# Kernel optimization log

Measured on AMD Instinct MI355X. Metric: run time of the kernel, lower is better.

Reference implementation:

```python
import jax, jax.numpy as jnp
import numpy as np
import math

D_MODEL = 768
NUM_HEADS = 12
D_K = D_MODEL // NUM_HEADS

def setup_inputs() -> dict:
    key = jax.random.key(0)
    k_x, k_q, k_k, k_v, k_o = jax.random.split(key, 5)
    x = jax.random.normal(k_x, (2, 2048, D_MODEL), dtype=jnp.float32)
    std = math.sqrt(2.0 / (D_MODEL + D_MODEL))
    # trunc_normal approx: clip normal to [-3std, 3std]
    def tn(k):
        return jnp.clip(jax.random.normal(k, (D_MODEL, D_MODEL), dtype=jnp.float32) * std, -3 * std, 3 * std)
    return {
        "x": x,
        "weight_query": tn(k_q),
        "weight_key": tn(k_k),
        "weight_value": tn(k_v),
        "weight_output": tn(k_o),
    }

def reference(x, weight_query, weight_key, weight_value, weight_output):
    # x: (b, s, d_model); weights: (d_out, d_model)
    b, s, _ = x.shape
    def proj_heads(w):
        y = jnp.einsum('od,bsd->bso', w, x)  # (b, s, h*dk)
        return y.reshape(b, s, NUM_HEADS, D_K).transpose(0, 2, 1, 3)  # (b, h, s, dk)
    Q = proj_heads(weight_query)
    K = proj_heads(weight_key)
    V = proj_heads(weight_value)
    scores = jnp.einsum('bhqd,bhkd->bhqk', Q, K) / jnp.sqrt(jnp.asarray(D_K, x.dtype))
    causal = jnp.tril(jnp.ones((s, s), dtype=bool))  # (sq, sk)
    scores = jnp.where(causal, scores, -jnp.inf)
    attn = jax.nn.softmax(scores, axis=-1)
    out_heads = jnp.einsum('bhqk,bhkd->bhqd', attn, V)  # (b, h, s, dv)
    attn_out = out_heads.transpose(0, 2, 1, 3).reshape(b, s, NUM_HEADS * D_K)
    return jnp.einsum('di,bsi->bsd', weight_output, attn_out)
```

## Files before the change

kernel.cpp:

```cpp
#include <hip/hip_runtime.h>
#include <stdint.h>

typedef float f32x4 __attribute__((ext_vector_type(4)));
typedef __bf16 bf16x8 __attribute__((ext_vector_type(8)));
typedef uint32_t u32a  __attribute__((may_alias));
typedef uint2    u2a   __attribute__((may_alias));
typedef uint4    u4a   __attribute__((may_alias));

#define VS 2064

__device__ __forceinline__ ushort f2b(float f) {
  uint32_t u = __builtin_bit_cast(uint32_t, f);
  u += 0x7FFFu + ((u >> 16) & 1u);
  return (ushort)(u >> 16);
}
__device__ __forceinline__ uint32_t b16(uint32_t u) {
  u += 0x7FFFu + ((u >> 16) & 1u);
  return u >> 16;
}

__device__ __forceinline__ bf16x8 ld_frag(const ushort* p) {
  u4a u = *(const u4a*)p;
  return __builtin_bit_cast(bf16x8, u);
}

__device__ __forceinline__ u4a cvt8(const float* p) {
  u4a a = *(const u4a*)p, b = *(const u4a*)(p + 4), o;
  o.x = b16(a.x) | (b16(a.y) << 16);
  o.y = b16(a.z) | (b16(a.w) << 16);
  o.z = b16(b.x) | (b16(b.y) << 16);
  o.w = b16(b.z) | (b16(b.w) << 16);
  return o;
}

__device__ __forceinline__ void load_lds16(const void* g, void* l) {
  __builtin_amdgcn_global_load_lds(
      (const __attribute__((address_space(1))) uint32_t*)g,
      (__attribute__((address_space(3))) uint32_t*)l, 16, 0, 0);
}

__device__ __forceinline__ uint32_t comb4(uint32_t a, uint32_t b, uint32_t c, uint32_t d,
                                          float w0, float w1, float w2, float w3) {
  float lo = __builtin_bit_cast(float, a << 16) * w0 +
             __builtin_bit_cast(float, b << 16) * w1 +
             __builtin_bit_cast(float, c << 16) * w2 +
             __builtin_bit_cast(float, d << 16) * w3;
  float hi = __builtin_bit_cast(float, a & 0xFFFF0000u) * w0 +
             __builtin_bit_cast(float, b & 0xFFFF0000u) * w1 +
             __builtin_bit_cast(float, c & 0xFFFF0000u) * w2 +
             __builtin_bit_cast(float, d & 0xFFFF0000u) * w3;
  return (uint32_t)f2b(lo) | ((uint32_t)f2b(hi) << 16);
}

__global__ __launch_bounds__(256) void convert_kernel(
    const float* __restrict__ x,  const float* __restrict__ wq,
    const float* __restrict__ wk, const float* __restrict__ wv,
    const float* __restrict__ wo,
    ushort* __restrict__ xb,  ushort* __restrict__ wqb,
    ushort* __restrict__ wkb, ushort* __restrict__ wvb,
    ushort* __restrict__ wob)
{
  const size_t NX = 3145728, NW = 589824;
  size_t idx = ((size_t)blockIdx.x * 256 + threadIdx.x) * 8;
  const float* src; ushort* dst; size_t off;
  if      (idx < NX)          { src = x;  dst = xb;  off = idx; }
  else if (idx < NX + NW)     { src = wq; dst = wqb; off = idx - NX; }
  else if (idx < NX + 2 * NW) { src = wk; dst = wkb; off = idx - NX - NW; }
  else if (idx < NX + 3 * NW) { src = wv; dst = wvb; off = idx - NX - 2 * NW; }
  else                        { src = wo; dst = wob; off = idx - NX - 3 * NW; }
  *(u4a*)(dst + off) = cvt8(src + off);
}

__global__ __launch_bounds__(256) void gemm_qkv(
    const ushort* __restrict__ A,
    const ushort* __restrict__ B0, const ushort* __restrict__ B1,
    const ushort* __restrict__ B2,
    ushort* __restrict__ Qo, ushort* __restrict__ Ko, ushort* __restrict__ Vt,
    int M, int N, int K)
{
  const ushort* B = blockIdx.z == 0 ? B0 : (blockIdx.z == 1 ? B1 : B2);
  const int m0 = blockIdx.x * 128, n0 = blockIdx.y * 64;
  __shared__ ushort As[128 * 64];
  __shared__ ushort Bs[64 * 64];
  const int tid = threadIdx.x, wave = tid >> 6, lane = tid & 63;
  const int quad = lane >> 4, l16 = lane & 15;
  const int mw = (wave & 1) * 64, nw = (wave >> 1) * 32;
  f32x4 acc[4][2] = {};

  for (int k0 = 0; k0 < K; k0 += 64) {
#pragma unroll
    for (int i = 0; i < 4; ++i) {
      int c = i * 256 + tid;
      load_lds16(A + (size_t)(m0 + (c >> 3)) * K + k0 + (c & 7) * 8,
                 As + (size_t)(i * 256 + wave * 64) * 8);
    }
#pragma unroll
    for (int i = 0; i < 2; ++i) {
      int c = i * 256 + tid;
      load_lds16(B + (size_t)(n0 + (c >> 3)) * K + k0 + (c & 7) * 8,
                 Bs + (size_t)(i * 256 + wave * 64) * 8);
    }
    __syncthreads();
#pragma unroll
    for (int ks = 0; ks < 2; ++ks) {
      bf16x8 af[4], bfr[2];
#pragma unroll
      for (int i = 0; i < 4; ++i)
        af[i]  = ld_frag(As + (mw + i * 16 + l16) * 64 + ks * 32 + quad * 8);
#pragma unroll
      for (int j = 0; j < 2; ++j)
        bfr[j] = ld_frag(Bs + (nw + j * 16 + l16) * 64 + ks * 32 + quad * 8);
#pragma unroll
      for (int i = 0; i < 4; ++i)
#pragma unroll
        for (int j = 0; j < 2; ++j)
          acc[i][j] = __builtin_amdgcn_mfma_f32_16x16x32_bf16(af[i], bfr[j], acc[i][j], 0, 0, 0);
    }
    __syncthreads();
  }
  if (blockIdx.z < 2) {
    ushort* C = blockIdx.z == 0 ? Qo : Ko;
    const float sc = blockIdx.z == 0 ? 0.18033688f : 1.0f;
#pragma unroll
    for (int i = 0; i < 4; ++i)
#pragma unroll
      for (int j = 0; j < 2; ++j)
#pragma unroll
        for (int r = 0; r < 4; ++r) {
          int row = m0 + mw + i * 16 + quad * 4 + r;
          int col = n0 + nw + j * 16 + l16;
          C[(size_t)row * N + col] = f2b(acc[i][j][r] * sc);
        }
  } else {
#pragma unroll
    for (int i = 0; i < 4; ++i)
#pragma unroll
      for (int j = 0; j < 2; ++j) {
        int col = n0 + nw + j * 16 + l16;
        int h = col >> 6, dv = col & 63;
        int t = m0 + mw + i * 16 + quad * 4;
        int b = t >> 11, s = t & 2047;
        u2a pw;
        pw.x = (uint32_t)f2b(acc[i][j][0]) | ((uint32_t)f2b(acc[i][j][1]) << 16);
        pw.y = (uint32_t)f2b(acc[i][j][2]) | ((uint32_t)f2b(acc[i][j][3]) << 16);
        *(u2a*)(Vt + (((size_t)b * 12 + h) * 64 + dv) * VS + s) = pw;
      }
  }
}

__global__ __launch_bounds__(256) void gemm_out(
    const ushort* __restrict__ A, const ushort* __restrict__ B,
    float* __restrict__ C, int M, int N, int K)
{
  const int m0 = blockIdx.x * 64, n0 = blockIdx.y * 64;
  __shared__ ushort As[64 * 64];
  __shared__ ushort Bs[64 * 64];
  const int tid = threadIdx.x, wave = tid >> 6, lane = tid & 63;
  const int quad = lane >> 4, l16 = lane & 15;
  const int mw = (wave & 1) * 32, nw = (wave >> 1) * 32;
  f32x4 acc[2][2] = {};

  for (int k0 = 0; k0 < K; k0 += 64) {
#pragma unroll
    for (int i = 0; i < 2; ++i) {
      int c = i * 256 + tid;
      load_lds16(A + (size_t)(m0 + (c >> 3)) * K + k0 + (c & 7) * 8,
                 As + (size_t)(i * 256 + wave * 64) * 8);
      load_lds16(B + (size_t)(n0 + (c >> 3)) * K + k0 + (c & 7) * 8,
                 Bs + (size_t)(i * 256 + wave * 64) * 8);
    }
    __syncthreads();
#pragma unroll
    for (int ks = 0; ks < 2; ++ks) {
      bf16x8 af[2], bfr[2];
#pragma unroll
      for (int i = 0; i < 2; ++i)
        af[i]  = ld_frag(As + (mw + i * 16 + l16) * 64 + ks * 32 + quad * 8);
#pragma unroll
      for (int j = 0; j < 2; ++j)
        bfr[j] = ld_frag(Bs + (nw + j * 16 + l16) * 64 + ks * 32 + quad * 8);
#pragma unroll
      for (int i = 0; i < 2; ++i)
#pragma unroll
        for (int j = 0; j < 2; ++j)
          acc[i][j] = __builtin_amdgcn_mfma_f32_16x16x32_bf16(af[i], bfr[j], acc[i][j], 0, 0, 0);
    }
    __syncthreads();
  }
#pragma unroll
  for (int i = 0; i < 2; ++i)
#pragma unroll
    for (int j = 0; j < 2; ++j)
#pragma unroll
      for (int r = 0; r < 4; ++r) {
        int row = m0 + mw + i * 16 + quad * 4 + r;
        int col = n0 + nw + j * 16 + l16;
        C[(size_t)row * N + col] = acc[i][j][r];
      }
}

__global__ __launch_bounds__(256) void attn_kernel(
    const ushort* __restrict__ Qb, const ushort* __restrict__ Kb,
    const ushort* __restrict__ Vt, ushort* __restrict__ Opart,
    float2* __restrict__ MLp)
{
  const int S = 2048, DM = 768;
  const int pair = blockIdx.x >> 2, j = blockIdx.x & 3;
  const int h = blockIdx.y, bb = blockIdx.z;
  const ushort* Qp  = Qb + (size_t)bb * S * DM + h * 64;
  const ushort* Kp  = Kb + (size_t)bb * S * DM + h * 64;
  const ushort* Vth = Vt + ((size_t)bb * 12 + h) * 64 * VS;

  __shared__ ushort Ks[64 * 72];
  __shared__ ushort Vs[64 * 72];

  const int tid = threadIdx.x, wave = tid >> 6, lane = tid & 63;
  const int quad = lane >> 4, l16 = lane & 15;
  const float NEG_BIG = -1.0e30f;

  const int qtA = pair, qtB = 31 - pair;
  const int qgA = qtA * 64 + wave * 16 + l16;
  const int qgB = qtB * 64 + wave * 16 + l16;

  bf16x8 bqA0 = ld_frag(Qp + (size_t)qgA * DM + quad * 8);
  bf16x8 bqA1 = ld_frag(Qp + (size_t)qgA * DM + 32 + quad * 8);
  bf16x8 bqB0 = ld_frag(Qp + (size_t)qgB * DM + quad * 8);
  bf16x8 bqB1 = ld_frag(Qp + (size_t)qgB * DM + 32 + quad * 8);

  f32x4 accA[4] = {}, accB[4] = {};
  float mA = NEG_BIG, lA = 0.0f, mB = NEG_BIG, lB = 0.0f;

  for (int kt = j; kt <= qtB; kt += 4) {
    const int kk0 = kt * 64;
#pragma unroll
    for (int i = 0; i < 2; ++i) {
      int c = i * 256 + tid;
      int r = c >> 3, col = (c & 7) * 8;
      *(u4a*)(Ks + r * 72 + col) = *(const u4a*)(Kp + (size_t)(kk0 + r) * DM + col);
    }
#pragma unroll
    for (int i = 0; i < 2; ++i) {
      int c = i * 256 + tid;
      int dv = c >> 3, kc8 = c & 7;
      u4a g = *(const u4a*)(Vth + (size_t)dv * VS + kk0 + kc8 * 8);
      int pos = ((kc8 >> 2) * 32) + ((kc8 & 1) * 16) + (((kc8 >> 1) & 1) * 4);
      u2a lo, hi;
      lo.x = g.x; lo.y = g.y; hi.x = g.z; hi.y = g.w;
      *(u2a*)(Vs + dv * 72 + pos)     = lo;
      *(u2a*)(Vs + dv * 72 + pos + 8) = hi;
    }
    __syncthreads();

    auto strip = [&](const bf16x8& bq0, const bf16x8& bq1, f32x4* acc_o,
                     float& m_run, float& l_run, int qg, int qt) {
      f32x4 sacc[4] = {};
#pragma unroll
      for (int tt = 0; tt < 4; ++tt) {
        bf16x8 ak0 = ld_frag(Ks + (tt * 16 + l16) * 72 + quad * 8);
        bf16x8 ak1 = ld_frag(Ks + (tt * 16 + l16) * 72 + 32 + quad * 8);
        sacc[tt] = __builtin_amdgcn_mfma_f32_16x16x32_bf16(ak0, bq0, sacc[tt], 0, 0, 0);
        sacc[tt] = __builtin_amdgcn_mfma_f32_16x16x32_bf16(ak1, bq1, sacc[tt], 0, 0, 0);
      }
      const bool domask = (kt == qt);
      float mt = NEG_BIG;
#pragma unroll
      for (int tt = 0; tt < 4; ++tt)
#pragma unroll
        for (int r = 0; r < 4; ++r) {
          float s = sacc[tt][r];
          if (domask) {
            int kkg = kk0 + tt * 16 + quad * 4 + r;
            if (kkg > qg) s = NEG_BIG;
          }
          sacc[tt][r] = s;
          mt = fmaxf(mt, s);
        }
      mt = fmaxf(mt, __shfl_xor(mt, 16, 64));
      mt = fmaxf(mt, __shfl_xor(mt, 32, 64));
      float mnew = fmaxf(m_run, mt);
      float alpha = exp2f(m_run - mnew);
      m_run = mnew;
      float ar0 = __shfl(alpha, quad * 4 + 0, 64);
      float ar1 = __shfl(alpha, quad * 4 + 1, 64);
      float ar2 = __shfl(alpha, quad * 4 + 2, 64);
      float ar3 = __shfl(alpha, quad * 4 + 3, 64);
#pragma unroll
      for (int ct = 0; ct < 4; ++ct) {
        acc_o[ct][0] *= ar0; acc_o[ct][1] *= ar1;
        acc_o[ct][2] *= ar2; acc_o[ct][3] *= ar3;
      }
      float lsum = 0.0f;
#pragma unroll
      for (int g = 0; g < 2; ++g) {
        u4a pu;
#pragma unroll
        for (int hlf = 0; hlf < 2; ++hlf) {
          int tt = g * 2 + hlf;
          float p0 = exp2f(sacc[tt][0] - mnew);
          float p1 = exp2f(sacc[tt][1] - mnew);
          float p2 = exp2f(sacc[tt][2] - mnew);
          float p3 = exp2f(sacc[tt][3] - mnew);
          lsum += (p0 + p1) + (p2 + p3);
          uint32_t u0 = __builtin_bit_cast(uint32_t, p0);
          uint32_t u1 = __builtin_bit_cast(uint32_t, p1);
          uint32_t u2 = __builtin_bit_cast(uint32_t, p2);
          uint32_t u3 = __builtin_bit_cast(uint32_t, p3);
          if (hlf == 0) {
            pu.x = (u0 >> 16) | (u1 & 0xFFFF0000u);
            pu.y = (u2 >> 16) | (u3 & 0xFFFF0000u);
          } else {
            pu.z = (u0 >> 16) | (u1 & 0xFFFF0000u);
            pu.w = (u2 >> 16) | (u3 & 0xFFFF0000u);
          }
        }
        bf16x8 ap = __builtin_bit_cast(bf16x8, pu);
#pragma unroll
        for (int ct = 0; ct < 4; ++ct) {
          bf16x8 bv = ld_frag(Vs + (size_t)(ct * 16 + l16) * 72 + g * 32 + quad * 8);
          acc_o[ct] = __builtin_amdgcn_mfma_f32_16x16x32_bf16(ap, bv, acc_o[ct], 0, 0, 0);
        }
      }
      lsum += __shfl_xor(lsum, 16, 64);
      lsum += __shfl_xor(lsum, 32, 64);
      l_run = l_run * alpha + lsum;
    };

    strip(bqB0, bqB1, accB, mB, lB, qgB, qtB);
    if (kt <= qtA)
      strip(bqA0, bqA1, accA, mA, lA, qgA, qtA);
    __syncthreads();
  }

  const int base = ((bb * 12 + h) << 5);
  const int r0 = wave * 16 + quad * 4;
  {
    const int slot = (base + qtB) * 4 + j;
    ushort* Os = Opart + (size_t)slot * 4096;
#pragma unroll
    for (int ct = 0; ct < 4; ++ct) {
      int col = ct * 16 + l16;
      Os[(r0 + 0) * 64 + col] = f2b(accB[ct][0]);
      Os[(r0 + 1) * 64 + col] = f2b(accB[ct][1]);
      Os[(r0 + 2) * 64 + col] = f2b(accB[ct][2]);
      Os[(r0 + 3) * 64 + col] = f2b(accB[ct][3]);
    }
    if (quad == 0)
      MLp[(size_t)slot * 64 + wave * 16 + l16] = make_float2(mB, lB);
  }
  {
    const int slot = (base + qtA) * 4 + j;
    ushort* Os = Opart + (size_t)slot * 4096;
#pragma unroll
    for (int ct = 0; ct < 4; ++ct) {
      int col = ct * 16 + l16;
      Os[(r0 + 0) * 64 + col] = f2b(accA[ct][0]);
      Os[(r0 + 1) * 64 + col] = f2b(accA[ct][1]);
      Os[(r0 + 2) * 64 + col] = f2b(accA[ct][2]);
      Os[(r0 + 3) * 64 + col] = f2b(accA[ct][3]);
    }
    if (quad == 0)
      MLp[(size_t)slot * 64 + wave * 16 + l16] = make_float2(mA, lA);
  }
}

__global__ __launch_bounds__(256) void combine_kernel(
    const ushort* __restrict__ Opart, const float2* __restrict__ MLp,
    ushort* __restrict__ Ab)
{
  const int sid = blockIdx.x;
  const int bb = sid / 384, rem = sid % 384, h = rem >> 5, qt = rem & 31;
  const int t = threadIdx.x, row = t >> 2, cg = (t & 3) * 16;
  float2 ml0 = MLp[(size_t)(sid * 4 + 0) * 64 + row];
  float2 ml1 = MLp[(size_t)(sid * 4 + 1) * 64 + row];
  float2 ml2 = MLp[(size_t)(sid * 4 + 2) * 64 + row];
  float2 ml3 = MLp[(size_t)(sid * 4 + 3) * 64 + row];
  float ms = fmaxf(fmaxf(ml0.x, ml1.x), fmaxf(ml2.x, ml3.x));
  float w0 = exp2f(ml0.x - ms);
  float w1 = exp2f(ml1.x - ms);
  float w2 = exp2f(ml2.x - ms);
  float w3 = exp2f(ml3.x - ms);
  float inv = 1.0f / (ml0.y * w0 + ml1.y * w1 + ml2.y * w2 + ml3.y * w3);
  w0 *= inv; w1 *= inv; w2 *= inv; w3 *= inv;
  const ushort* p0 = Opart + (size_t)(sid * 4) * 4096 + row * 64 + cg;
  ushort* dst = Ab + ((size_t)(bb * 2048 + qt * 64 + row)) * 768 + h * 64 + cg;
#pragma unroll
  for (int g = 0; g < 2; ++g) {
    u4a a = *(const u4a*)(p0 + g * 8);
    u4a b = *(const u4a*)(p0 + 4096 + g * 8);
    u4a c = *(const u4a*)(p0 + 8192 + g * 8);
    u4a d = *(const u4a*)(p0 + 12288 + g * 8);
    u4a o;
    o.x = comb4(a.x, b.x, c.x, d.x, w0, w1, w2, w3);
    o.y = comb4(a.y, b.y, c.y, d.y, w0, w1, w2, w3);
    o.z = comb4(a.z, b.z, c.z, d.z, w0, w1, w2, w3);
    o.w = comb4(a.w, b.w, c.w, d.w, w0, w1, w2, w3);
    *(u4a*)(dst + g * 8) = o;
  }
}

extern "C" void kernel_launch(void* const* d_in, const int* in_sizes, int n_in,
                              void* d_out, int out_size, void* d_ws, size_t ws_size,
                              hipStream_t stream) {
  (void)in_sizes; (void)n_in; (void)out_size; (void)ws_size;
  const float* x  = (const float*)d_in[0];
  const float* wq = (const float*)d_in[1];
  const float* wk = (const float*)d_in[2];
  const float* wv = (const float*)d_in[3];
  const float* wo = (const float*)d_in[4];

  const size_t NT = (size_t)4096 * 768;
  const size_t NW = (size_t)768 * 768;
  const size_t NV = (size_t)24 * 64 * VS;
  ushort* xb    = (ushort*)d_ws;
  ushort* Qbuf  = xb + NT;
  ushort* Kbuf  = Qbuf + NT;
  ushort* Vt    = Kbuf + NT;
  ushort* wqb   = Vt + NV;
  ushort* wkb   = wqb + NW;
  ushort* wvb   = wkb + NW;
  ushort* wob   = wvb + NW;
  ushort* Opart = wob + NW;
  float2* MLp   = (float2*)(Opart + (size_t)3072 * 4096);
  ushort* Abuf  = xb;

  convert_kernel<<<2688, 256, 0, stream>>>(x, wq, wk, wv, wo,
                                           xb, wqb, wkb, wvb, wob);
  gemm_qkv<<<dim3(32, 12, 3), 256, 0, stream>>>(
      xb, wqb, wkb, wvb, Qbuf, Kbuf, Vt, 4096, 768, 768);
  attn_kernel<<<dim3(64, 12, 2), 256, 0, stream>>>(Qbuf, Kbuf, Vt, Opart, MLp);
  combine_kernel<<<768, 256, 0, stream>>>(Opart, MLp, Abuf);
  gemm_out<<<dim3(64, 12), 256, 0, stream>>>(
      Abuf, wob, (float*)d_out, 4096, 768, 768);
}
```

Baseline: 172.3 us.

## Double-buffer K/V tiles, raise KV split to 8, and skip small rescales

The attention kernel now double-buffers K/V tiles in shared memory, loading the next tile into registers while the current one is computed, which removes one barrier per iteration. The KV split count rises from 4 to 8 when the workspace is large enough, giving more blocks and less serial work per block, and the combine kernel loops over a variable number of partials. Online-softmax rescaling is skipped unless some row max grows by more than 8 (lazy rescale). The cost is more partial-output traffic and combine work, and the larger LDS footprint may lower occupancy.

Measured after the change: 192.1 us. 1.11x slower.

```diff
diff --git a/kernel.cpp b/kernel.cpp
--- a/kernel.cpp
+++ b/kernel.cpp
@@ -17,6 +17,12 @@
 __device__ __forceinline__ uint32_t b16(uint32_t u) {
   u += 0x7FFFu + ((u >> 16) & 1u);
   return u >> 16;
+}
+__device__ __forceinline__ float blo(uint32_t a) {
+  return __builtin_bit_cast(float, a << 16);
+}
+__device__ __forceinline__ float bhi(uint32_t a) {
+  return __builtin_bit_cast(float, a & 0xFFFF0000u);
 }
 
 __device__ __forceinline__ bf16x8 ld_frag(const ushort* p) {
@@ -37,19 +43,6 @@
   __builtin_amdgcn_global_load_lds(
       (const __attribute__((address_space(1))) uint32_t*)g,
       (__attribute__((address_space(3))) uint32_t*)l, 16, 0, 0);
-}
-
-__device__ __forceinline__ uint32_t comb4(uint32_t a, uint32_t b, uint32_t c, uint32_t d,
-                                          float w0, float w1, float w2, float w3) {
-  float lo = __builtin_bit_cast(float, a << 16) * w0 +
-             __builtin_bit_cast(float, b << 16) * w1 +
-             __builtin_bit_cast(float, c << 16) * w2 +
-             __builtin_bit_cast(float, d << 16) * w3;
-  float hi = __builtin_bit_cast(float, a & 0xFFFF0000u) * w0 +
-             __builtin_bit_cast(float, b & 0xFFFF0000u) * w1 +
-             __builtin_bit_cast(float, c & 0xFFFF0000u) * w2 +
-             __builtin_bit_cast(float, d & 0xFFFF0000u) * w3;
-  return (uint32_t)f2b(lo) | ((uint32_t)f2b(hi) << 16);
 }
 
 __global__ __launch_bounds__(256) void convert_kernel(
@@ -202,17 +195,18 @@
 __global__ __launch_bounds__(256) void attn_kernel(
     const ushort* __restrict__ Qb, const ushort* __restrict__ Kb,
     const ushort* __restrict__ Vt, ushort* __restrict__ Opart,
-    float2* __restrict__ MLp)
+    float2* __restrict__ MLp, int sl)
 {
   const int S = 2048, DM = 768;
-  const int pair = blockIdx.x >> 2, j = blockIdx.x & 3;
+  const int split = 1 << sl;
+  const int pair = blockIdx.x >> sl, j = blockIdx.x & (split - 1);
   const int h = blockIdx.y, bb = blockIdx.z;
   const ushort* Qp  = Qb + (size_t)bb * S * DM + h * 64;
   const ushort* Kp  = Kb + (size_t)bb * S * DM + h * 64;
   const ushort* Vth = Vt + ((size_t)bb * 12 + h) * 64 * VS;
 
-  __shared__ ushort Ks[64 * 72];
-  __shared__ ushort Vs[64 * 72];
+  __shared__ ushort Ks[2][64 * 72];
+  __shared__ ushort Vs[2][64 * 72];
 
   const int tid = threadIdx.x, wave = tid >> 6, lane = tid & 63;
   const int quad = lane >> 4, l16 = lane & 15;
@@ -230,38 +224,57 @@
   f32x4 accA[4] = {}, accB[4] = {};
   float mA = NEG_BIG, lA = 0.0f, mB = NEG_BIG, lB = 0.0f;
 
-  for (int kt = j; kt <= qtB; kt += 4) {
-    const int kk0 = kt * 64;
+  u4a kr[2], vr[2];
+
+  {
+    const int kk0 = j * 64;
 #pragma unroll
     for (int i = 0; i < 2; ++i) {
       int c = i * 256 + tid;
-      int r = c >> 3, col = (c & 7) * 8;
-      *(u4a*)(Ks + r * 72 + col) = *(const u4a*)(Kp + (size_t)(kk0 + r) * DM + col);
+      kr[i] = *(const u4a*)(Kp + (size_t)(kk0 + (c >> 3)) * DM + (c & 7) * 8);
+      vr[i] = *(const u4a*)(Vth + (size_t)(c >> 3) * VS + kk0 + (c & 7) * 8);
     }
 #pragma unroll
     for (int i = 0; i < 2; ++i) {
       int c = i * 256 + tid;
+      *(u4a*)(&Ks[0][(c >> 3) * 72 + (c & 7) * 8]) = kr[i];
       int dv = c >> 3, kc8 = c & 7;
-      u4a g = *(const u4a*)(Vth + (size_t)dv * VS + kk0 + kc8 * 8);
       int pos = ((kc8 >> 2) * 32) + ((kc8 & 1) * 16) + (((kc8 >> 1) & 1) * 4);
       u2a lo, hi;
-      lo.x = g.x; lo.y = g.y; hi.x = g.z; hi.y = g.w;
-      *(u2a*)(Vs + dv * 72 + pos)     = lo;
-      *(u2a*)(Vs + dv * 72 + pos + 8) = hi;
-    }
-    __syncthreads();
+      lo.x = vr[i].x; lo.y = vr[i].y; hi.x = vr[i].z; hi.y = vr[i].w;
+      *(u2a*)(&Vs[0][dv * 72 + pos])     = lo;
+      *(u2a*)(&Vs[0][dv * 72 + pos + 8]) = hi;
+    }
+  }
+  __syncthreads();
+
+  int cur = 0;
+  for (int kt = j; kt <= qtB; kt += split) {
+    const int kk0 = kt * 64;
+    const int nx = kt + split;
+    const bool hasNext = (nx <= qtB);
+    if (hasNext) {
+      const int nk0 = nx * 64;
+#pragma unroll
+      for (int i = 0; i < 2; ++i) {
+        int c = i * 256 + tid;
+        kr[i] = *(const u4a*)(Kp + (size_t)(nk0 + (c >> 3)) * DM + (c & 7) * 8);
+        vr[i] = *(const u4a*)(Vth + (size_t)(c >> 3) * VS + nk0 + (c & 7) * 8);
+      }
+    }
+    const ushort* Kc = &Ks[cur][0];
+    const ushort* Vc = &Vs[cur][0];
 
     auto strip = [&](const bf16x8& bq0, const bf16x8& bq1, f32x4* acc_o,
-                     float& m_run, float& l_run, int qg, int qt) {
+                     float& m_run, float& l_run, int qg, bool domask) {
       f32x4 sacc[4] = {};
 #pragma unroll
       for (int tt = 0; tt < 4; ++tt) {
-        bf16x8 ak0 = ld_frag(Ks + (tt * 16 + l16) * 72 + quad * 8);
-        bf16x8 ak1 = ld_frag(Ks + (tt * 16 + l16) * 72 + 32 + quad * 8);
+        bf16x8 ak0 = ld_frag(Kc + (tt * 16 + l16) * 72 + quad * 8);
+        bf16x8 ak1 = ld_frag(Kc + (tt * 16 + l16) * 72 + 32 + quad * 8);
         sacc[tt] = __builtin_amdgcn_mfma_f32_16x16x32_bf16(ak0, bq0, sacc[tt], 0, 0, 0);
         sacc[tt] = __builtin_amdgcn_mfma_f32_16x16x32_bf16(ak1, bq1, sacc[tt], 0, 0, 0);
       }
-      const bool domask = (kt == qt);
       float mt = NEG_BIG;
 #pragma unroll
       for (int tt = 0; tt < 4; ++tt)
@@ -277,18 +290,22 @@
         }
       mt = fmaxf(mt, __shfl_xor(mt, 16, 64));
       mt = fmaxf(mt, __shfl_xor(mt, 32, 64));
-      float mnew = fmaxf(m_run, mt);
-      float alpha = exp2f(m_run - mnew);
-      m_run = mnew;
-      float ar0 = __shfl(alpha, quad * 4 + 0, 64);
-      float ar1 = __shfl(alpha, quad * 4 + 1, 64);
-      float ar2 = __shfl(alpha, quad * 4 + 2, 64);
-      float ar3 = __shfl(alpha, quad * 4 + 3, 64);
-#pragma unroll
-      for (int ct = 0; ct < 4; ++ct) {
-        acc_o[ct][0] *= ar0; acc_o[ct][1] *= ar1;
-        acc_o[ct][2] *= ar2; acc_o[ct][3] *= ar3;
-      }
+      if (__any(mt > m_run + 8.0f)) {
+        float mnew = fmaxf(m_run, mt);
+        float alpha = exp2f(m_run - mnew);
+        m_run = mnew;
+        float ar0 = __shfl(alpha, quad * 4 + 0, 64);
+        float ar1 = __shfl(alpha, quad * 4 + 1, 64);
+        float ar2 = __shfl(alpha, quad * 4 + 2, 64);
+        float ar3 = __shfl(alpha, quad * 4 + 3, 64);
+#pragma unroll
+        for (int ct = 0; ct < 4; ++ct) {
+          acc_o[ct][0] *= ar0; acc_o[ct][1] *= ar1;
+          acc_o[ct][2] *= ar2; acc_o[ct][3] *= ar3;
+        }
+        l_run *= alpha;
+      }
+      const float mnew = m_run;
       float lsum = 0.0f;
 #pragma unroll
       for (int g = 0; g < 2; ++g) {
@@ -316,25 +333,42 @@
         bf16x8 ap = __builtin_bit_cast(bf16x8, pu);
 #pragma unroll
         for (int ct = 0; ct < 4; ++ct) {
-          bf16x8 bv = ld_frag(Vs + (size_t)(ct * 16 + l16) * 72 + g * 32 + quad * 8);
+          bf16x8 bv = ld_frag(Vc + (size_t)(ct * 16 + l16) * 72 + g * 32 + quad * 8);
           acc_o[ct] = __builtin_amdgcn_mfma_f32_16x16x32_bf16(ap, bv, acc_o[ct], 0, 0, 0);
         }
       }
       lsum += __shfl_xor(lsum, 16, 64);
       lsum += __shfl_xor(lsum, 32, 64);
-      l_run = l_run * alpha + lsum;
+      l_run += lsum;
     };
 
-    strip(bqB0, bqB1, accB, mB, lB, qgB, qtB);
+    strip(bqB0, bqB1, accB, mB, lB, qgB, kt == qtB);
     if (kt <= qtA)
-      strip(bqA0, bqA1, accA, mA, lA, qgA, qtA);
+      strip(bqA0, bqA1, accA, mA, lA, qgA, kt == qtA);
+
+    if (hasNext) {
+      ushort* Kn = &Ks[cur ^ 1][0];
+      ushort* Vn = &Vs[cur ^ 1][0];
+#pragma unroll
+      for (int i = 0; i < 2; ++i) {
+        int c = i * 256 + tid;
+        *(u4a*)(&Kn[(c >> 3) * 72 + (c & 7) * 8]) = kr[i];
+        int dv = c >> 3, kc8 = c & 7;
+        int pos = ((kc8 >> 2) * 32) + ((kc8 & 1) * 16) + (((kc8 >> 1) & 1) * 4);
+        u2a lo, hi;
+        lo.x = vr[i].x; lo.y = vr[i].y; hi.x = vr[i].z; hi.y = vr[i].w;
+        *(u2a*)(&Vn[dv * 72 + pos])     = lo;
+        *(u2a*)(&Vn[dv * 72 + pos + 8]) = hi;
+      }
+    }
     __syncthreads();
+    cur ^= 1;
   }
 
   const int base = ((bb * 12 + h) << 5);
   const int r0 = wave * 16 + quad * 4;
   {
-    const int slot = (base + qtB) * 4 + j;
+    const int slot = (base + qtB) * split + j;
     ushort* Os = Opart + (size_t)slot * 4096;
 #pragma unroll
     for (int ct = 0; ct < 4; ++ct) {
@@ -348,7 +382,7 @@
       MLp[(size_t)slot * 64 + wave * 16 + l16] = make_float2(mB, lB);
   }
   {
-    const int slot = (base + qtA) * 4 + j;
+    const int slot = (base + qtA) * split + j;
     ushort* Os = Opart + (size_t)slot * 4096;
 #pragma unroll
     for (int ct = 0; ct < 4; ++ct) {
@@ -365,35 +399,42 @@
 
 __global__ __launch_bounds__(256) void combine_kernel(
     const ushort* __restrict__ Opart, const float2* __restrict__ MLp,
-    ushort* __restrict__ Ab)
+    ushort* __restrict__ Ab, int split)
 {
   const int sid = blockIdx.x;
   const int bb = sid / 384, rem = sid % 384, h = rem >> 5, qt = rem & 31;
   const int t = threadIdx.x, row = t >> 2, cg = (t & 3) * 16;
-  float2 ml0 = MLp[(size_t)(sid * 4 + 0) * 64 + row];
-  float2 ml1 = MLp[(size_t)(sid * 4 + 1) * 64 + row];
-  float2 ml2 = MLp[(size_t)(sid * 4 + 2) * 64 + row];
-  float2 ml3 = MLp[(size_t)(sid * 4 + 3) * 64 + row];
-  float ms = fmaxf(fmaxf(ml0.x, ml1.x), fmaxf(ml2.x, ml3.x));
-  float w0 = exp2f(ml0.x - ms);
-  float w1 = exp2f(ml1.x - ms);
-  float w2 = exp2f(ml2.x - ms);
-  float w3 = exp2f(ml3.x - ms);
-  float inv = 1.0f / (ml0.y * w0 + ml1.y * w1 + ml2.y * w2 + ml3.y * w3);
-  w0 *= inv; w1 *= inv; w2 *= inv; w3 *= inv;
-  const ushort* p0 = Opart + (size_t)(sid * 4) * 4096 + row * 64 + cg;
+  const float2* mlp = MLp + (size_t)sid * split * 64 + row;
+  float ms = -1.0e30f;
+  for (int i = 0; i < split; ++i) ms = fmaxf(ms, mlp[(size_t)i * 64].x);
+  float denom = 0.0f;
+  for (int i = 0; i < split; ++i) {
+    float2 ml = mlp[(size_t)i * 64];
+    denom += ml.y * exp2f(ml.x - ms);
+  }
+  const float inv = 1.0f / denom;
+  float os[16] = {};
+  const ushort* p0 = Opart + (size_t)sid * split * 4096 + row * 64 + cg;
+  for (int i = 0; i < split; ++i) {
+    float2 ml = mlp[(size_t)i * 64];
+    float w = exp2f(ml.x - ms) * inv;
+#pragma unroll
+    for (int g = 0; g < 2; ++g) {
+      u4a a = *(const u4a*)(p0 + (size_t)i * 4096 + g * 8);
+      os[g * 8 + 0] += blo(a.x) * w; os[g * 8 + 1] += bhi(a.x) * w;
+      os[g * 8 + 2] += blo(a.y) * w; os[g * 8 + 3] += bhi(a.y) * w;
+      os[g * 8 + 4] += blo(a.z) * w; os[g * 8 + 5] += bhi(a.z) * w;
+      os[g * 8 + 6] += blo(a.w) * w; os[g * 8 + 7] += bhi(a.w) * w;
+    }
+  }
   ushort* dst = Ab + ((size_t)(bb * 2048 + qt * 64 + row)) * 768 + h * 64 + cg;
 #pragma unroll
   for (int g = 0; g < 2; ++g) {
-    u4a a = *(const u4a*)(p0 + g * 8);
-    u4a b = *(const u4a*)(p0 + 4096 + g * 8);
-    u4a c = *(const u4a*)(p0 + 8192 + g * 8);
-    u4a d = *(const u4a*)(p0 + 12288 + g * 8);
     u4a o;
-    o.x = comb4(a.x, b.x, c.x, d.x, w0, w1, w2, w3);
-    o.y = comb4(a.y, b.y, c.y, d.y, w0, w1, w2, w3);
-    o.z = comb4(a.z, b.z, c.z, d.z, w0, w1, w2, w3);
-    o.w = comb4(a.w, b.w, c.w, d.w, w0, w1, w2, w3);
+    o.x = (uint32_t)f2b(os[g * 8 + 0]) | ((uint32_t)f2b(os[g * 8 + 1]) << 16);
+    o.y = (uint32_t)f2b(os[g * 8 + 2]) | ((uint32_t)f2b(os[g * 8 + 3]) << 16);
+    o.z = (uint32_t)f2b(os[g * 8 + 4]) | ((uint32_t)f2b(os[g * 8 + 5]) << 16);
+    o.w = (uint32_t)f2b(os[g * 8 + 6]) | ((uint32_t)f2b(os[g * 8 + 7]) << 16);
     *(u4a*)(dst + g * 8) = o;
   }
 }
@@ -401,7 +442,7 @@
 extern "C" void kernel_launch(void* const* d_in, const int* in_sizes, int n_in,
                               void* d_out, int out_size, void* d_ws, size_t ws_size,
                               hipStream_t stream) {
-  (void)in_sizes; (void)n_in; (void)out_size; (void)ws_size;
+  (void)in_sizes; (void)n_in; (void)out_size;
   const float* x  = (const float*)d_in[0];
   const float* wq = (const float*)d_in[1];
   const float* wk = (const float*)d_in[2];
@@ -411,6 +452,15 @@
   const size_t NT = (size_t)4096 * 768;
   const size_t NW = (size_t)768 * 768;
   const size_t NV = (size_t)24 * 64 * VS;
+  const size_t usBase = 3 * NT + NV + 4 * NW;
+
+  int sl = 3, split = 8;
+  {
+    size_t need = 2 * (usBase + (size_t)768 * 8 * 4096) +
+                  (size_t)768 * 8 * 64 * sizeof(float2);
+    if (ws_size && ws_size < need) { sl = 2; split = 4; }
+  }
+
   ushort* xb    = (ushort*)d_ws;
   ushort* Qbuf  = xb + NT;
   ushort* Kbuf  = Qbuf + NT;
@@ -420,15 +470,16 @@
   ushort* wvb   = wkb + NW;
   ushort* wob   = wvb + NW;
   ushort* Opart = wob + NW;
-  float2* MLp   = (float2*)(Opart + (size_t)3072 * 4096);
+  float2* MLp   = (float2*)(Opart + (size_t)768 * split * 4096);
   ushort* Abuf  = xb;
 
   convert_kernel<<<2688, 256, 0, stream>>>(x, wq, wk, wv, wo,
                                            xb, wqb, wkb, wvb, wob);
   gemm_qkv<<<dim3(32, 12, 3), 256, 0, stream>>>(
       xb, wqb, wkb, wvb, Qbuf, Kbuf, Vt, 4096, 768, 768);
-  attn_kernel<<<dim3(64, 12, 2), 256, 0, stream>>>(Qbuf, Kbuf, Vt, Opart, MLp);
-  combine_kernel<<<768, 256, 0, stream>>>(Opart, MLp, Abuf);
+  attn_kernel<<<dim3(16 * split, 12, 2), 256, 0, stream>>>(
+      Qbuf, Kbuf, Vt, Opart, MLp, sl);
+  combine_kernel<<<768, 256, 0, stream>>>(Opart, MLp, Abuf, split);
   gemm_out<<<dim3(64, 12), 256, 0, stream>>>(
       Abuf, wob, (float*)d_out, 4096, 768, 768);
 }
```
